# Kernel tuning notes

Hardware: AMD Instinct MI355X
Metric: run time of the kernel (lower is better)

Reference implementation:

```python
import jax, jax.numpy as jnp
import numpy as np

DIM = 256
HEADS = 8
WIN = (8, 8)
DQ = 4   # num_frames_q
DKV = 4  # num_frames_kv
N1 = DQ * WIN[0] * WIN[1]   # 256
N2 = DKV * WIN[0] * WIN[1]  # 256
B_ = 256   # B * nW
NW = 128   # windows per batch element


def _rel_pos_index():
    # mirrors WindowAttention3D.__init__ (torch.meshgrid default indexing='ij')
    coords_d_q = np.arange(DQ)
    step = (DQ + 1) // DKV
    if step != 0:
        coords_d_kv = np.arange(0, DQ, step)
    else:
        coords_d_kv = np.zeros(DKV, dtype=np.int64)
    ch = np.arange(WIN[0])
    cw = np.arange(WIN[1])
    cq = np.stack(np.meshgrid(coords_d_q, ch, cw, indexing='ij'))   # (3, DQ, Wh, Ww)
    ckv = np.stack(np.meshgrid(coords_d_kv, ch, cw, indexing='ij'))
    qf = cq.reshape(3, -1)   # (3, N1)
    kf = ckv.reshape(3, -1)  # (3, N2)
    rel = (qf[:, :, None] - kf[:, None, :]).transpose(1, 2, 0)  # (N1, N2, 3)
    rel[..., 0] += DQ - 1
    rel[..., 1] += WIN[0] - 1
    rel[..., 2] += WIN[1] - 1
    rel[..., 0] *= (2 * WIN[0] - 1) * (2 * WIN[1] - 1)
    rel[..., 1] *= 2 * WIN[1] - 1
    return rel.sum(-1)  # (N1, N2)


def setup_inputs() -> dict:
    key = jax.random.key(0)
    ks = jax.random.split(key, 10)
    table_sz = (2 * DQ - 1) * (2 * WIN[0] - 1) * (2 * WIN[1] - 1)  # 1575
    inp = {
        'q': jax.random.normal(ks[0], (B_, N1, DIM), jnp.float32),
        'kv': jax.random.normal(ks[1], (B_, N2, DIM), jnp.float32),
        'mask': jax.random.normal(ks[2], (NW, N1, N2), jnp.float32),
        'Wq': jax.random.normal(ks[3], (DIM, DIM), jnp.float32) * 0.02,
        'bq': jnp.zeros((DIM,), jnp.float32),
        'Wkv': jax.random.normal(ks[4], (2 * DIM, DIM), jnp.float32) * 0.02,
        'bkv': jnp.zeros((2 * DIM,), jnp.float32),
        'bias_table': jax.random.normal(ks[5], (table_sz, HEADS), jnp.float32) * 0.02,
        'Wp': jax.random.normal(ks[6], (DIM, DIM), jnp.float32) * 0.02,
        'bp': jnp.zeros((DIM,), jnp.float32),
        'rel_index': jnp.asarray(_rel_pos_index(), jnp.int32),
    }
    return inp


def reference(q, kv, mask, Wq, bq, Wkv, bkv, bias_table, Wp, bp, rel_index):
    B, n1, C = q.shape
    n2 = kv.shape[1]
    hd = C // HEADS
    scale = hd ** -0.5
    # projections
    qh = (q @ Wq.T + bq).reshape(B, n1, HEADS, hd).transpose(0, 2, 1, 3)      # (B,H,N1,hd)
    kvh = (kv @ Wkv.T + bkv).reshape(B, n2, 2, HEADS, hd).transpose(2, 0, 3, 1, 4)
    k, v = kvh[0], kvh[1]                                                      # (B,H,N2,hd)
    attn = jnp.einsum('bhqd,bhkd->bhqk', qh * scale, k)                        # (B,H,N1,N2)
    # relative position bias gather
    bias = bias_table[rel_index]                                               # (N1,N2,H)
    attn = attn + bias.transpose(2, 0, 1)[None]
    # shift mask (nW, N1, N2) broadcast over batch and heads
    nW = mask.shape[0]
    attn = attn.reshape(B // nW, nW, HEADS, n1, n2) + mask[None, :, None]
    attn = jax.nn.softmax(attn.reshape(B, HEADS, n1, n2), axis=-1)
    x = jnp.einsum('bhqk,bhkd->bqhd', attn, v).reshape(B, n1, C)
    x = x @ Wp.T + bp
    return x
```

## Files before the change

kernel.cpp:

```cpp
#include <hip/hip_runtime.h>

#define BH_TOTAL 2048
#define SCALE_Q 0.17677669529663687f

typedef unsigned short ushort;
typedef unsigned int uint;
typedef __attribute__((ext_vector_type(8))) short bf16x8;
typedef __attribute__((ext_vector_type(4))) ushort u16x4;
typedef __attribute__((ext_vector_type(4))) float f32x4;

static __device__ __forceinline__ ushort f2bf(float f) {
    union { float f; uint u; } v; v.f = f;
    uint r = (v.u + 0x7fffu + ((v.u >> 16) & 1u)) >> 16;
    return (ushort)r;
}
static __device__ __forceinline__ ushort bfru(float f) {
    union { float f; uint u; } v; v.f = f;
    return (ushort)((v.u + 0x8000u) >> 16);
}
static __device__ __forceinline__ float bflo(uint w) {
    union { uint u; float f; } v; v.u = w << 16; return v.f;
}
static __device__ __forceinline__ float bfhi(uint w) {
    union { uint u; float f; } v; v.u = w & 0xffff0000u; return v.f;
}

__global__ __launch_bounds__(256)
void cvt_all(const float* __restrict__ q, const float* __restrict__ kv,
             const float* __restrict__ Wq, const float* __restrict__ Wkv,
             const float* __restrict__ Wp,
             ushort* __restrict__ qb, ushort* __restrict__ kvb,
             ushort* __restrict__ wqb, ushort* __restrict__ wkvb,
             ushort* __restrict__ wpb)
{
    const int bid = blockIdx.x, tid = threadIdx.x;
    const float* src; ushort* dst; int base;
    if (bid < 8192)       { src = q;   dst = qb;   base = bid; }
    else if (bid < 16384) { src = kv;  dst = kvb;  base = bid - 8192; }
    else if (bid < 16416) { src = Wq;  dst = wqb;  base = bid - 16384; }
    else if (bid < 16480) { src = Wkv; dst = wkvb; base = bid - 16416; }
    else                  { src = Wp;  dst = wpb;  base = bid - 16480; }
    size_t off = ((size_t)base * 256 + tid) * 8;
    float4 a = *(const float4*)&src[off];
    float4 b = *(const float4*)&src[off + 4];
    bf16x8 p = {(short)f2bf(a.x), (short)f2bf(a.y), (short)f2bf(a.z), (short)f2bf(a.w),
                (short)f2bf(b.x), (short)f2bf(b.y), (short)f2bf(b.z), (short)f2bf(b.w)};
    *(bf16x8*)&dst[off] = p;
}

__global__ __launch_bounds__(256)
void mask_pre(const float* __restrict__ mask, ushort* __restrict__ maskP)
{
    __shared__ float rows[1024];
    const int w = blockIdx.x >> 6, qb = blockIdx.x & 63;
    const int tid = threadIdx.x;
    const float* src = mask + (size_t)w * 65536 + qb * 1024;
    #pragma unroll
    for (int i = 0; i < 4; ++i) rows[tid + 256 * i] = src[tid + 256 * i];
    __syncthreads();
    const int jt = tid & 15, col = tid >> 4;
    u16x4 p;
    #pragma unroll
    for (int r = 0; r < 4; ++r) p[r] = f2bf(rows[r * 256 + jt * 16 + col]);
    *(u16x4*)&maskP[(size_t)w * 65536 + qb * 1024 + tid * 4] = p;
}

__global__ __launch_bounds__(256)
void bias_pre(const float* __restrict__ bias_table, const int* __restrict__ rel_index,
              float* __restrict__ biasF)
{
    __shared__ int idx[1024];
    const int h = blockIdx.x >> 6, qb = blockIdx.x & 63;
    const int tid = threadIdx.x;
    const int* src = rel_index + qb * 1024;
    #pragma unroll
    for (int i = 0; i < 4; ++i) idx[tid + 256 * i] = src[tid + 256 * i];
    __syncthreads();
    const int jt = tid & 15, col = tid >> 4;
    f32x4 p;
    #pragma unroll
    for (int r = 0; r < 4; ++r)
        p[r] = bias_table[idx[r * 256 + jt * 16 + col] * 8 + h];
    *(f32x4*)&biasF[(size_t)h * 65536 + qb * 1024 + tid * 4] = p;
}

template<int MODE>
__global__ __launch_bounds__(256)
void gemm_mfma(const ushort* __restrict__ A, const ushort* __restrict__ W,
               const float* __restrict__ bias, float* __restrict__ outf,
               ushort* __restrict__ outh0, ushort* __restrict__ outh1)
{
    __shared__ ushort As[128 * 72];
    __shared__ ushort Bs[128 * 72];

    const int tid  = threadIdx.x;
    const int n0   = blockIdx.x * 128;
    const int m0   = blockIdx.y * 128;
    const int lane = tid & 63, wave = tid >> 6;
    const int col  = lane & 15, quad = lane >> 4;
    const int wm   = (wave >> 1) * 64, wn = (wave & 1) * 64;

    f32x4 acc[4][4];
    #pragma unroll
    for (int i = 0; i < 4; ++i)
        #pragma unroll
        for (int j = 0; j < 4; ++j)
            acc[i][j] = (f32x4){0.f, 0.f, 0.f, 0.f};

    for (int k0 = 0; k0 < 256; k0 += 64) {
        __syncthreads();
        #pragma unroll
        for (int i = 0; i < 4; ++i) {
            int f = tid + 256 * i;
            int row = f >> 3, c8 = f & 7;
            *(bf16x8*)&As[row * 72 + c8 * 8] =
                *(const bf16x8*)&A[(size_t)(m0 + row) * 256 + k0 + c8 * 8];
        }
        #pragma unroll
        for (int i = 0; i < 4; ++i) {
            int f = tid + 256 * i;
            int row = f >> 3, c8 = f & 7;
            *(bf16x8*)&Bs[row * 72 + c8 * 8] =
                *(const bf16x8*)&W[(size_t)(n0 + row) * 256 + k0 + c8 * 8];
        }
        __syncthreads();
        #pragma unroll
        for (int ks = 0; ks < 64; ks += 32) {
            bf16x8 af[4], bfr[4];
            #pragma unroll
            for (int t = 0; t < 4; ++t) {
                af[t]  = *(const bf16x8*)&As[(wm + t * 16 + col) * 72 + ks + quad * 8];
                bfr[t] = *(const bf16x8*)&Bs[(wn + t * 16 + col) * 72 + ks + quad * 8];
            }
            #pragma unroll
            for (int mt = 0; mt < 4; ++mt)
                #pragma unroll
                for (int nt = 0; nt < 4; ++nt)
                    acc[mt][nt] = __builtin_amdgcn_mfma_f32_16x16x32_bf16(
                        af[mt], bfr[nt], acc[mt][nt], 0, 0, 0);
        }
    }

    #pragma unroll
    for (int mt = 0; mt < 4; ++mt) {
        const int mb = m0 + wm + mt * 16 + quad * 4;
        #pragma unroll
        for (int nt = 0; nt < 4; ++nt) {
            const int n = n0 + wn + nt * 16 + col;
            const float bn = bias[n];
            if (MODE == 1 && n >= 256) {
                const int nn = n - 256;
                const int b = mb >> 8, m1 = mb & 255;
                u16x4 p;
                #pragma unroll
                for (int r = 0; r < 4; ++r)
                    p[r] = f2bf(acc[mt][nt][r] + bn);
                *(u16x4*)&outh1[(size_t)((b << 3) | (nn >> 5)) * 8192
                                + (nn & 31) * 256 + m1] = p;
            } else {
                #pragma unroll
                for (int r = 0; r < 4; ++r) {
                    int m = mb + r;
                    int b = m >> 8, m1 = m & 255;
                    float v = acc[mt][nt][r] + bn;
                    if (MODE == 0) {
                        outh0[(size_t)((b << 3) | (n >> 5)) * 8192 + m1 * 32 + (n & 31)]
                            = f2bf(v * SCALE_Q);
                    } else if (MODE == 1) {
                        outh0[(size_t)((b << 3) | (n >> 5)) * 8192 + m1 * 32 + (n & 31)]
                            = f2bf(v);
                    } else {
                        outf[(size_t)m * 256 + n] = v;
                    }
                }
            }
        }
    }
}

__global__ __launch_bounds__(256)
void attn_mfma(const ushort* __restrict__ qh, const ushort* __restrict__ kb,
               const ushort* __restrict__ vt, const ushort* __restrict__ maskP,
               const float* __restrict__ biasF, ushort* __restrict__ xbuf)
{
    __shared__ ushort Ks[256 * 40];
    __shared__ ushort Vts[32 * 264];
    __shared__ ushort Ps[4][16 * 264];

    const int g  = blockIdx.x;
    const int w  = g >> 4;
    const int b2 = (g >> 3) & 1, h = g & 7;
    const int b  = b2 * 128 + w;
    const int bh = b * 8 + h;

    const int tid  = threadIdx.x;
    const int lane = tid & 63, wave = tid >> 6;
    const int col  = lane & 15;
    const int quad = lane >> 4;

    const ushort* __restrict__ Qg  = qh + (size_t)bh * 8192;
    const ushort* __restrict__ Kg  = kb + (size_t)bh * 8192;
    const ushort* __restrict__ Vg  = vt + (size_t)bh * 8192;
    const ushort* __restrict__ MgP = maskP + (size_t)w * 65536;
    const float*  __restrict__ BgF = biasF + (size_t)h * 65536;

    for (int t = tid; t < 1024; t += 256) {
        int j = t >> 2, p = t & 3;
        *(bf16x8*)&Ks[j * 40 + p * 8] = *(const bf16x8*)&Kg[j * 32 + p * 8];
    }
    for (int t = tid; t < 1024; t += 256) {
        int d = t >> 5, p = t & 31;
        *(bf16x8*)&Vts[d * 264 + p * 8] = *(const bf16x8*)&Vg[d * 256 + p * 8];
    }
    __syncthreads();

    ushort* __restrict__ Pw = &Ps[wave][0];
    const f32x4 zero = {0.f, 0.f, 0.f, 0.f};

    for (int it = 0; it < 4; ++it) {
        const int q0 = (wave * 4 + it) * 16;
        const int qb = (q0 >> 2) + quad;

        const ushort* mp  = &MgP[(size_t)(qb * 16 + col) * 64];
        const float*  bp2 = &BgF[(size_t)(qb * 16 + col) * 64];
        uint4 mq[8];
        #pragma unroll
        for (int i = 0; i < 8; ++i) mq[i] = *(const uint4*)&mp[i * 8];

        bf16x8 aq = *(const bf16x8*)&Qg[(q0 + col) * 32 + quad * 8];
        f32x4 acc[16];
        #pragma unroll
        for (int jt = 0; jt < 16; ++jt) {
            f32x4 bv = *(const f32x4*)&bp2[jt * 4];
            uint u0, u1;
            if (jt & 1) { u0 = mq[jt >> 1].z; u1 = mq[jt >> 1].w; }
            else        { u0 = mq[jt >> 1].x; u1 = mq[jt >> 1].y; }
            f32x4 c;
            c[0] = bv[0] + bflo(u0);
            c[1] = bv[1] + bfhi(u0);
            c[2] = bv[2] + bflo(u1);
            c[3] = bv[3] + bfhi(u1);
            bf16x8 bk = *(const bf16x8*)&Ks[(jt * 16 + col) * 40 + quad * 8];
            acc[jt] = __builtin_amdgcn_mfma_f32_16x16x32_bf16(aq, bk, c, 0, 0, 0);
        }

        float mx[4], sm[4], inv[4];
        #pragma unroll
        for (int r = 0; r < 4; ++r) {
            float m = acc[0][r];
            #pragma unroll
            for (int jt = 1; jt < 16; ++jt) m = fmaxf(m, acc[jt][r]);
            #pragma unroll
            for (int off = 1; off < 16; off <<= 1) m = fmaxf(m, __shfl_xor(m, off));
            mx[r] = m;
            sm[r] = 0.f;
        }
        #pragma unroll
        for (int jt = 0; jt < 16; ++jt) {
            #pragma unroll
            for (int r = 0; r < 4; ++r) {
                float e = __expf(acc[jt][r] - mx[r]);
                acc[jt][r] = e;
                sm[r] += e;
            }
        }
        #pragma unroll
        for (int r = 0; r < 4; ++r) {
            float s = sm[r];
            #pragma unroll
            for (int off = 1; off < 16; off <<= 1) s += __shfl_xor(s, off);
            inv[r] = 1.0f / s;
        }

        #pragma unroll
        for (int jt = 0; jt < 16; ++jt) {
            #pragma unroll
            for (int r = 0; r < 4; ++r)
                Pw[(quad * 4 + r) * 264 + jt * 16 + col] = bfru(acc[jt][r]);
        }

        f32x4 x0 = zero, x1 = zero;
        #pragma unroll
        for (int kc = 0; kc < 8; ++kc) {
            bf16x8 ap  = *(const bf16x8*)&Pw[col * 264 + kc * 32 + quad * 8];
            bf16x8 bv0 = *(const bf16x8*)&Vts[col * 264 + kc * 32 + quad * 8];
            bf16x8 bv1 = *(const bf16x8*)&Vts[(col + 16) * 264 + kc * 32 + quad * 8];
            x0 = __builtin_amdgcn_mfma_f32_16x16x32_bf16(ap, bv0, x0, 0, 0, 0);
            x1 = __builtin_amdgcn_mfma_f32_16x16x32_bf16(ap, bv1, x1, 0, 0, 0);
        }

        #pragma unroll
        for (int r = 0; r < 4; ++r) {
            int row = q0 + quad * 4 + r;
            size_t base = (size_t)(b * 256 + row) * 256 + h * 32;
            xbuf[base + col]      = f2bf(x0[r] * inv[r]);
            xbuf[base + 16 + col] = f2bf(x1[r] * inv[r]);
        }
    }
}

extern "C" void kernel_launch(void* const* d_in, const int* in_sizes, int n_in,
                              void* d_out, int out_size, void* d_ws, size_t ws_size,
                              hipStream_t stream)
{
    const float* q          = (const float*)d_in[0];
    const float* kv         = (const float*)d_in[1];
    const float* mask       = (const float*)d_in[2];
    const float* Wq         = (const float*)d_in[3];
    const float* bq         = (const float*)d_in[4];
    const float* Wkv        = (const float*)d_in[5];
    const float* bkv        = (const float*)d_in[6];
    const float* bias_table = (const float*)d_in[7];
    const float* Wp         = (const float*)d_in[8];
    const float* bp         = (const float*)d_in[9];
    const int*   rel_index  = (const int*)d_in[10];
    float* out = (float*)d_out;

    char* ws = (char*)d_ws;
    ushort* qhb   = (ushort*)(ws);
    ushort* qb16  = (ushort*)(ws + (size_t)33554432);
    ushort* kbb   = (ushort*)(ws + (size_t)33554432);
    ushort* vtb   = (ushort*)(ws + (size_t)67108864);
    ushort* kvb16 = (ushort*)(ws + (size_t)100663296);
    ushort* xb    = (ushort*)(ws + (size_t)100663296);
    ushort* mP    = (ushort*)(ws + (size_t)134217728);
    float*  bF    = (float*) (ws + (size_t)150994944);
    ushort* wqb   = (ushort*)(ws + (size_t)153092096);
    ushort* wkvb  = (ushort*)(ws + (size_t)153223168);
    ushort* wpb   = (ushort*)(ws + (size_t)153485312);

    dim3 blk(256);
    cvt_all<<<dim3(16512), blk, 0, stream>>>(q, kv, Wq, Wkv, Wp,
                                             qb16, kvb16, wqb, wkvb, wpb);
    mask_pre<<<dim3(8192), blk, 0, stream>>>(mask, mP);
    bias_pre<<<dim3(512),  blk, 0, stream>>>(bias_table, rel_index, bF);
    gemm_mfma<0><<<dim3(2, 512), blk, 0, stream>>>(qb16,  wqb,  bq,  nullptr, qhb, nullptr);
    gemm_mfma<1><<<dim3(4, 512), blk, 0, stream>>>(kvb16, wkvb, bkv, nullptr, kbb, vtb);
    attn_mfma<<<dim3(BH_TOTAL), blk, 0, stream>>>(qhb, kbb, vtb, mP, bF, xb);
    gemm_mfma<2><<<dim3(2, 512), blk, 0, stream>>>(xb, wpb, bp, out, nullptr, nullptr);
}
```

Measured before the change: 432.2 us.

## Transpose QK^T MFMA to keep softmax probabilities in registers, drop LDS P buffer

Computes S^T with K as the A operand, so each lane holds a full query row's scores. That makes row max and sum mostly in-register reductions, and P can be packed directly into MFMA A fragments for the PV product. This removes the per-wave LDS staging buffer for P. Mask and bias are re-laid out (bias now stored as bf16), and V's key order is permuted to match the new fragment ordering. It also adds an occupancy hint; the cost is register pressure and extra bf16 rounding of the bias.

After: 552.1 us. 1.28x slower.

```diff
diff --git a/kernel.cpp b/kernel.cpp
--- a/kernel.cpp
+++ b/kernel.cpp
@@ -58,16 +58,21 @@
     #pragma unroll
     for (int i = 0; i < 4; ++i) rows[tid + 256 * i] = src[tid + 256 * i];
     __syncthreads();
-    const int jt = tid & 15, col = tid >> 4;
+    const int row = tid >> 6;
+    const int ib  = (tid & 63) * 4;
     u16x4 p;
     #pragma unroll
-    for (int r = 0; r < 4; ++r) p[r] = f2bf(rows[r * 256 + jt * 16 + col]);
-    *(u16x4*)&maskP[(size_t)w * 65536 + qb * 1024 + tid * 4] = p;
+    for (int r = 0; r < 4; ++r) {
+        int i = ib + r;
+        int j = ((i >> 2) & 15) * 16 + (i >> 6) * 4 + (i & 3);
+        p[r] = f2bf(rows[row * 256 + j]);
+    }
+    *(u16x4*)&maskP[(size_t)w * 65536 + (qb * 4 + row) * 256 + ib] = p;
 }
 
 __global__ __launch_bounds__(256)
 void bias_pre(const float* __restrict__ bias_table, const int* __restrict__ rel_index,
-              float* __restrict__ biasF)
+              ushort* __restrict__ biasP)
 {
     __shared__ int idx[1024];
     const int h = blockIdx.x >> 6, qb = blockIdx.x & 63;
@@ -76,12 +81,16 @@
     #pragma unroll
     for (int i = 0; i < 4; ++i) idx[tid + 256 * i] = src[tid + 256 * i];
     __syncthreads();
-    const int jt = tid & 15, col = tid >> 4;
-    f32x4 p;
-    #pragma unroll
-    for (int r = 0; r < 4; ++r)
-        p[r] = bias_table[idx[r * 256 + jt * 16 + col] * 8 + h];
-    *(f32x4*)&biasF[(size_t)h * 65536 + qb * 1024 + tid * 4] = p;
+    const int row = tid >> 6;
+    const int ib  = (tid & 63) * 4;
+    u16x4 p;
+    #pragma unroll
+    for (int r = 0; r < 4; ++r) {
+        int i = ib + r;
+        int j = ((i >> 2) & 15) * 16 + (i >> 6) * 4 + (i & 3);
+        p[r] = f2bf(bias_table[idx[row * 256 + j] * 8 + h]);
+    }
+    *(u16x4*)&biasP[(size_t)h * 65536 + (qb * 4 + row) * 256 + ib] = p;
 }
 
 template<int MODE>
@@ -151,12 +160,13 @@
             if (MODE == 1 && n >= 256) {
                 const int nn = n - 256;
                 const int b = mb >> 8, m1 = mb & 255;
+                const int m1p = (m1 & 0xE3) | ((m1 & 0x0C) << 1) | ((m1 & 0x10) >> 2);
                 u16x4 p;
                 #pragma unroll
                 for (int r = 0; r < 4; ++r)
                     p[r] = f2bf(acc[mt][nt][r] + bn);
                 *(u16x4*)&outh1[(size_t)((b << 3) | (nn >> 5)) * 8192
-                                + (nn & 31) * 256 + m1] = p;
+                                + (nn & 31) * 256 + m1p] = p;
             } else {
                 #pragma unroll
                 for (int r = 0; r < 4; ++r) {
@@ -178,14 +188,13 @@
     }
 }
 
-__global__ __launch_bounds__(256)
+__global__ __launch_bounds__(256, 4)
 void attn_mfma(const ushort* __restrict__ qh, const ushort* __restrict__ kb,
                const ushort* __restrict__ vt, const ushort* __restrict__ maskP,
-               const float* __restrict__ biasF, ushort* __restrict__ xbuf)
+               const ushort* __restrict__ biasP, ushort* __restrict__ xbuf)
 {
     __shared__ ushort Ks[256 * 40];
     __shared__ ushort Vts[32 * 264];
-    __shared__ ushort Ps[4][16 * 264];
 
     const int g  = blockIdx.x;
     const int w  = g >> 4;
@@ -198,11 +207,11 @@
     const int col  = lane & 15;
     const int quad = lane >> 4;
 
-    const ushort* __restrict__ Qg  = qh + (size_t)bh * 8192;
-    const ushort* __restrict__ Kg  = kb + (size_t)bh * 8192;
-    const ushort* __restrict__ Vg  = vt + (size_t)bh * 8192;
-    const ushort* __restrict__ MgP = maskP + (size_t)w * 65536;
-    const float*  __restrict__ BgF = biasF + (size_t)h * 65536;
+    const ushort* __restrict__ Qg = qh + (size_t)bh * 8192;
+    const ushort* __restrict__ Kg = kb + (size_t)bh * 8192;
+    const ushort* __restrict__ Vg = vt + (size_t)bh * 8192;
+    const ushort* __restrict__ Mg = maskP + (size_t)w * 65536;
+    const ushort* __restrict__ Bg = biasP + (size_t)h * 65536;
 
     for (int t = tid; t < 1024; t += 256) {
         int j = t >> 2, p = t & 3;
@@ -214,87 +223,106 @@
     }
     __syncthreads();
 
-    ushort* __restrict__ Pw = &Ps[wave][0];
     const f32x4 zero = {0.f, 0.f, 0.f, 0.f};
 
     for (int it = 0; it < 4; ++it) {
-        const int q0 = (wave * 4 + it) * 16;
-        const int qb = (q0 >> 2) + quad;
-
-        const ushort* mp  = &MgP[(size_t)(qb * 16 + col) * 64];
-        const float*  bp2 = &BgF[(size_t)(qb * 16 + col) * 64];
-        uint4 mq[8];
-        #pragma unroll
-        for (int i = 0; i < 8; ++i) mq[i] = *(const uint4*)&mp[i * 8];
-
-        bf16x8 aq = *(const bf16x8*)&Qg[(q0 + col) * 32 + quad * 8];
+        const int q0   = (wave * 4 + it) * 16;
+        const int qrow = q0 + col;
+
+        const ushort* mp  = &Mg[(size_t)qrow * 256 + quad * 64];
+        const ushort* bp2 = &Bg[(size_t)qrow * 256 + quad * 64];
+
+        bf16x8 fq = *(const bf16x8*)&Qg[(size_t)qrow * 32 + quad * 8];
+
         f32x4 acc[16];
         #pragma unroll
         for (int jt = 0; jt < 16; ++jt) {
-            f32x4 bv = *(const f32x4*)&bp2[jt * 4];
-            uint u0, u1;
-            if (jt & 1) { u0 = mq[jt >> 1].z; u1 = mq[jt >> 1].w; }
-            else        { u0 = mq[jt >> 1].x; u1 = mq[jt >> 1].y; }
-            f32x4 c;
-            c[0] = bv[0] + bflo(u0);
-            c[1] = bv[1] + bfhi(u0);
-            c[2] = bv[2] + bflo(u1);
-            c[3] = bv[3] + bfhi(u1);
-            bf16x8 bk = *(const bf16x8*)&Ks[(jt * 16 + col) * 40 + quad * 8];
-            acc[jt] = __builtin_amdgcn_mfma_f32_16x16x32_bf16(aq, bk, c, 0, 0, 0);
-        }
-
-        float mx[4], sm[4], inv[4];
-        #pragma unroll
-        for (int r = 0; r < 4; ++r) {
-            float m = acc[0][r];
-            #pragma unroll
-            for (int jt = 1; jt < 16; ++jt) m = fmaxf(m, acc[jt][r]);
-            #pragma unroll
-            for (int off = 1; off < 16; off <<= 1) m = fmaxf(m, __shfl_xor(m, off));
-            mx[r] = m;
-            sm[r] = 0.f;
-        }
+            bf16x8 fk = *(const bf16x8*)&Ks[(jt * 16 + col) * 40 + quad * 8];
+            acc[jt] = __builtin_amdgcn_mfma_f32_16x16x32_bf16(fk, fq, zero, 0, 0, 0);
+        }
+
+        #pragma unroll
+        for (int half = 0; half < 2; ++half) {
+            uint4 mw[4], bw[4];
+            #pragma unroll
+            for (int i = 0; i < 4; ++i) {
+                mw[i] = *(const uint4*)(mp  + half * 32 + i * 8);
+                bw[i] = *(const uint4*)(bp2 + half * 32 + i * 8);
+            }
+            #pragma unroll
+            for (int jt8 = 0; jt8 < 8; ++jt8) {
+                const int jt = half * 8 + jt8;
+                uint4 mv4 = mw[jt8 >> 1];
+                uint4 bv4 = bw[jt8 >> 1];
+                uint mu0 = (jt8 & 1) ? mv4.z : mv4.x;
+                uint mu1 = (jt8 & 1) ? mv4.w : mv4.y;
+                uint bu0 = (jt8 & 1) ? bv4.z : bv4.x;
+                uint bu1 = (jt8 & 1) ? bv4.w : bv4.y;
+                acc[jt][0] += bflo(mu0) + bflo(bu0);
+                acc[jt][1] += bfhi(mu0) + bfhi(bu0);
+                acc[jt][2] += bflo(mu1) + bflo(bu1);
+                acc[jt][3] += bfhi(mu1) + bfhi(bu1);
+            }
+        }
+
+        float mv[16];
+        #pragma unroll
+        for (int jt = 0; jt < 16; ++jt)
+            mv[jt] = fmaxf(fmaxf(acc[jt][0], acc[jt][1]),
+                           fmaxf(acc[jt][2], acc[jt][3]));
+        #pragma unroll
+        for (int st = 8; st >= 1; st >>= 1)
+            #pragma unroll
+            for (int i = 0; i < 8; ++i)
+                if (i < st) mv[i] = fmaxf(mv[i], mv[i + st]);
+        float m = mv[0];
+        m = fmaxf(m, __shfl_xor(m, 16));
+        m = fmaxf(m, __shfl_xor(m, 32));
+
+        float sv[16];
         #pragma unroll
         for (int jt = 0; jt < 16; ++jt) {
             #pragma unroll
             for (int r = 0; r < 4; ++r) {
-                float e = __expf(acc[jt][r] - mx[r]);
+                float e = __expf(acc[jt][r] - m);
                 acc[jt][r] = e;
-                sm[r] += e;
-            }
-        }
-        #pragma unroll
-        for (int r = 0; r < 4; ++r) {
-            float s = sm[r];
-            #pragma unroll
-            for (int off = 1; off < 16; off <<= 1) s += __shfl_xor(s, off);
-            inv[r] = 1.0f / s;
-        }
-
-        #pragma unroll
-        for (int jt = 0; jt < 16; ++jt) {
-            #pragma unroll
-            for (int r = 0; r < 4; ++r)
-                Pw[(quad * 4 + r) * 264 + jt * 16 + col] = bfru(acc[jt][r]);
-        }
+            }
+            sv[jt] = (acc[jt][0] + acc[jt][1]) + (acc[jt][2] + acc[jt][3]);
+        }
+        #pragma unroll
+        for (int st = 8; st >= 1; st >>= 1)
+            #pragma unroll
+            for (int i = 0; i < 8; ++i)
+                if (i < st) sv[i] += sv[i + st];
+        float s = sv[0];
+        s += __shfl_xor(s, 16);
+        s += __shfl_xor(s, 32);
+        const float inv = 1.0f / s;
+
+        bf16x8 pa[8];
+        #pragma unroll
+        for (int kc = 0; kc < 8; ++kc)
+            #pragma unroll
+            for (int t2 = 0; t2 < 2; ++t2)
+                #pragma unroll
+                for (int r = 0; r < 4; ++r)
+                    pa[kc][t2 * 4 + r] = (short)bfru(acc[kc * 2 + t2][r] * inv);
 
         f32x4 x0 = zero, x1 = zero;
         #pragma unroll
         for (int kc = 0; kc < 8; ++kc) {
-            bf16x8 ap  = *(const bf16x8*)&Pw[col * 264 + kc * 32 + quad * 8];
             bf16x8 bv0 = *(const bf16x8*)&Vts[col * 264 + kc * 32 + quad * 8];
             bf16x8 bv1 = *(const bf16x8*)&Vts[(col + 16) * 264 + kc * 32 + quad * 8];
-            x0 = __builtin_amdgcn_mfma_f32_16x16x32_bf16(ap, bv0, x0, 0, 0, 0);
-            x1 = __builtin_amdgcn_mfma_f32_16x16x32_bf16(ap, bv1, x1, 0, 0, 0);
+            x0 = __builtin_amdgcn_mfma_f32_16x16x32_bf16(pa[kc], bv0, x0, 0, 0, 0);
+            x1 = __builtin_amdgcn_mfma_f32_16x16x32_bf16(pa[kc], bv1, x1, 0, 0, 0);
         }
 
         #pragma unroll
         for (int r = 0; r < 4; ++r) {
             int row = q0 + quad * 4 + r;
             size_t base = (size_t)(b * 256 + row) * 256 + h * 32;
-            xbuf[base + col]      = f2bf(x0[r] * inv[r]);
-            xbuf[base + 16 + col] = f2bf(x1[r] * inv[r]);
+            xbuf[base + col]      = f2bf(x0[r]);
+            xbuf[base + 16 + col] = f2bf(x1[r]);
         }
     }
 }
@@ -324,7 +352,7 @@
     ushort* kvb16 = (ushort*)(ws + (size_t)100663296);
     ushort* xb    = (ushort*)(ws + (size_t)100663296);
     ushort* mP    = (ushort*)(ws + (size_t)134217728);
-    float*  bF    = (float*) (ws + (size_t)150994944);
+    ushort* bP    = (ushort*)(ws + (size_t)150994944);
     ushort* wqb   = (ushort*)(ws + (size_t)153092096);
     ushort* wkvb  = (ushort*)(ws + (size_t)153223168);
     ushort* wpb   = (ushort*)(ws + (size_t)153485312);
@@ -333,9 +361,9 @@
     cvt_all<<<dim3(16512), blk, 0, stream>>>(q, kv, Wq, Wkv, Wp,
                                              qb16, kvb16, wqb, wkvb, wpb);
     mask_pre<<<dim3(8192), blk, 0, stream>>>(mask, mP);
-    bias_pre<<<dim3(512),  blk, 0, stream>>>(bias_table, rel_index, bF);
+    bias_pre<<<dim3(512),  blk, 0, stream>>>(bias_table, rel_index, bP);
     gemm_mfma<0><<<dim3(2, 512), blk, 0, stream>>>(qb16,  wqb,  bq,  nullptr, qhb, nullptr);
     gemm_mfma<1><<<dim3(4, 512), blk, 0, stream>>>(kvb16, wkvb, bkv, nullptr, kbb, vtb);
-    attn_mfma<<<dim3(BH_TOTAL), blk, 0, stream>>>(qhb, kbb, vtb, mP, bF, xb);
+    attn_mfma<<<dim3(BH_TOTAL), blk, 0, stream>>>(qhb, kbb, vtb, mP, bP, xb);
     gemm_mfma<2><<<dim3(2, 512), blk, 0, stream>>>(xb, wpb, bp, out, nullptr, nullptr);
 }
```
